# Kernel tuning notes

Hardware: AMD Instinct MI355X
Metric: run time of the kernel (lower is better)

## Reference

```python
import jax, jax.numpy as jnp
import numpy as np

D = 1024          # input_dim == output_dim (module requires this)
H = 4 * D         # expert hidden dim
E = 8             # num_experts
TOP_K = 2
N = 16384         # tokens


def setup_inputs() -> dict:
    key = jax.random.key(0)
    ks = jax.random.split(key, 8)
    s = 0.02
    return {
        "x": jax.random.normal(ks[0], (N, D), dtype=jnp.float32),
        "grad": jax.random.normal(ks[1], (N, 1), dtype=jnp.float32),
        "rW": jax.random.normal(ks[2], (D + 1, E), dtype=jnp.float32) * s,
        "rb": jnp.zeros((E,), dtype=jnp.float32),
        "W1": jax.random.normal(ks[3], (E, D, H), dtype=jnp.float32) * s,
        "b1": jnp.zeros((E, H), dtype=jnp.float32),
        "W2": jax.random.normal(ks[4], (E, H, D), dtype=jnp.float32) * s,
        "b2": jnp.zeros((E, D), dtype=jnp.float32),
    }


def reference(x, grad, rW, rb, W1, b1, W2, b2):
    # Router over [x, grad]
    logits = jnp.concatenate([x, grad], axis=-1) @ rW + rb          # [N, E]
    probs = jax.nn.softmax(logits, axis=-1)                          # [N, E]
    topk_probs, topk_idx = jax.lax.top_k(probs, TOP_K)               # [N, K]
    # Dense gate matrix: gate[n, e] = topk prob if e selected else 0
    gates = jnp.zeros_like(probs).at[jnp.arange(x.shape[0])[:, None], topk_idx].add(topk_probs)
    # Combine: out = sum_e gate_e * MLP_e(x). Dropout is identity at eval.
    out = jnp.zeros((x.shape[0], D), dtype=x.dtype)
    for e in range(E):  # fixed small loop over experts
        h = jax.nn.gelu(x @ W1[e] + b1[e], approximate=False)        # [N, H]
        y = h @ W2[e] + b2[e]                                        # [N, D]
        out = out + gates[:, e:e + 1] * y
    return out, probs
```

## Files before the change

### kernel.cpp

```cpp
#include <hip/hip_runtime.h>
#include <hip/hip_bf16.h>
#include <math.h>

#define NTOK 16384
#define DDIM 1024
#define HDIM 4096
#define NEXP 8

typedef __bf16 bf16_t;
typedef __bf16 bf16x8 __attribute__((ext_vector_type(8)));
typedef float f32x4 __attribute__((ext_vector_type(4)));

__device__ __forceinline__ void gld16(const bf16_t* g, bf16_t* l) {
    __builtin_amdgcn_global_load_lds(
        (const __attribute__((address_space(1))) void*)g,
        (__attribute__((address_space(3))) void*)l, 16, 0, 0);
}

__device__ __forceinline__ void stage_half(const bf16_t* __restrict__ g, int K, int kofs,
                                           bf16_t* l, int tid) {
#pragma unroll
    for (int c = 0; c < 2; ++c) {
        const int s = c * 512 + tid;
        const int kg = s >> 7, r = s & 127;
        gld16(g + (size_t)r * K + (kofs + kg * 8), l + (size_t)s * 8);
    }
}


__global__ void init_counts(int* counts) {
    if (threadIdx.x < NEXP) counts[threadIdx.x] = 0;
}

__global__ void router_kernel(const float* __restrict__ x, const float* __restrict__ grad,
                              const float* __restrict__ rW, const float* __restrict__ rb,
                              float* __restrict__ probs, int* __restrict__ t2i,
                              float* __restrict__ t2g, int* __restrict__ counts) {
    const int lane = threadIdx.x & 63;
    const int n = blockIdx.x * 4 + (threadIdx.x >> 6);
    float acc[NEXP];
#pragma unroll
    for (int e = 0; e < NEXP; ++e) acc[e] = 0.f;
    const float* xr = x + (size_t)n * DDIM;
    for (int d = lane; d < DDIM; d += 64) {
        float xv = xr[d];
        const float* rr = rW + (size_t)d * NEXP;
#pragma unroll
        for (int e = 0; e < NEXP; ++e) acc[e] = fmaf(xv, rr[e], acc[e]);
    }
#pragma unroll
    for (int e = 0; e < NEXP; ++e) {
#pragma unroll
        for (int off = 32; off > 0; off >>= 1)
            acc[e] += __shfl_xor(acc[e], off, 64);
    }
    if (lane == 0) {
        float gv = grad[n];
        float p[NEXP];
        float mx = -1e30f;
#pragma unroll
        for (int e = 0; e < NEXP; ++e) {
            p[e] = acc[e] + gv * rW[(size_t)DDIM * NEXP + e] + rb[e];
            mx = fmaxf(mx, p[e]);
        }
        float s = 0.f;
#pragma unroll
        for (int e = 0; e < NEXP; ++e) { p[e] = expf(p[e] - mx); s += p[e]; }
        float inv = 1.f / s;
        int i1 = 0; float v1 = -1.f;
#pragma unroll
        for (int e = 0; e < NEXP; ++e) {
            p[e] *= inv;
            probs[(size_t)n * NEXP + e] = p[e];
            if (p[e] > v1) { v1 = p[e]; i1 = e; }
        }
        int i2 = 0; float v2 = -2.f;
#pragma unroll
        for (int e = 0; e < NEXP; ++e) {
            if (e != i1 && p[e] > v2) { v2 = p[e]; i2 = e; }
        }
        t2i[n * 2] = i1; t2i[n * 2 + 1] = i2;
        t2g[n * 2] = v1; t2g[n * 2 + 1] = v2;
        atomicAdd(&counts[i1], 1);
        atomicAdd(&counts[i2], 1);
    }
}

__global__ void offsets_kernel(const int* __restrict__ counts, int* __restrict__ offsets,
                               int* __restrict__ cursor) {
    if (threadIdx.x == 0) {
        int s = 0;
        for (int e = 0; e < NEXP; ++e) { offsets[e] = s; cursor[e] = s; s += counts[e]; }
    }
}

__global__ void build_lists(const int* __restrict__ t2i, const float* __restrict__ t2g,
                            int* __restrict__ cursor, int* __restrict__ tok,
                            float* __restrict__ gate, int* __restrict__ tslot) {
    int n = blockIdx.x * 256 + threadIdx.x;
#pragma unroll
    for (int k = 0; k < 2; ++k) {
        int e = t2i[n * 2 + k];
        int slot = atomicAdd(&cursor[e], 1);
        tok[slot] = n;
        gate[slot] = t2g[n * 2 + k];
        tslot[n * 2 + k] = slot;
    }
}

__global__ void gather_kernel(const float* __restrict__ x, const int* __restrict__ tok,
                              bf16_t* __restrict__ Xg) {
    const int r = blockIdx.x;
    const int t = threadIdx.x;
    const int token = tok[r];
    float4 v = ((const float4*)(x + (size_t)token * DDIM))[t];
    bf16_t o[4] = { (bf16_t)v.x, (bf16_t)v.y, (bf16_t)v.z, (bf16_t)v.w };
    *(uint2*)(Xg + (size_t)r * DDIM + t * 4) = *(const uint2*)o;
}

__global__ void transpose_cast(const float* __restrict__ in, bf16_t* __restrict__ out,
                               int R, int C) {
    __shared__ float tile[32][33];
    const size_t ebase = (size_t)blockIdx.z * R * C;
    const int c0 = blockIdx.x * 32, r0 = blockIdx.y * 32;
    const int tx = threadIdx.x, ty = threadIdx.y;
#pragma unroll
    for (int j = 0; j < 32; j += 8)
        tile[ty + j][tx] = in[ebase + (size_t)(r0 + ty + j) * C + c0 + tx];
    __syncthreads();
#pragma unroll
    for (int j = 0; j < 32; j += 8)
        out[ebase + (size_t)(c0 + ty + j) * R + r0 + tx] = (bf16_t)tile[tx][ty + j];
}

__global__ void combine_kernel(const float* __restrict__ Yg, const int* __restrict__ tslot,
                               float* __restrict__ out) {
    const int n = blockIdx.x, t = threadIdx.x;
    const int s1 = tslot[n * 2], s2 = tslot[n * 2 + 1];
    const float4 a = ((const float4*)(Yg + (size_t)s1 * DDIM))[t];
    const float4 b = ((const float4*)(Yg + (size_t)s2 * DDIM))[t];
    ((float4*)(out + (size_t)n * DDIM))[t] =
        make_float4(a.x + b.x, a.y + b.y, a.z + b.z, a.w + b.w);
}

#define PHASE_SYNC() do { \
    __builtin_amdgcn_s_barrier(); \
    asm volatile("s_waitcnt lgkmcnt(0)" ::: "memory"); \
    __builtin_amdgcn_sched_barrier(0); \
    __builtin_amdgcn_s_setprio(1); \
} while (0)

#define PHASE_END() do { \
    __builtin_amdgcn_s_setprio(0); \
    __builtin_amdgcn_s_barrier(); \
} while (0)

#define MMA16(QA, QB) do { \
    _Pragma("unroll") \
    for (int mt = 0; mt < 4; ++mt) { \
        _Pragma("unroll") \
        for (int nt = 0; nt < 2; ++nt) { \
            _Pragma("unroll") \
            for (int ks = 0; ks < 2; ++ks) \
                acc[(QA) * 4 + mt][(QB) * 2 + nt] = \
                    __builtin_amdgcn_mfma_f32_16x16x32_bf16( \
                        aF[mt][ks], bF[nt][ks], acc[(QA) * 4 + mt][(QB) * 2 + nt], 0, 0, 0); \
        } \
    } \
} while (0)

template <int K, int EPI>
__global__ __launch_bounds__(512, 2)
void moe_gemm8(const bf16_t* __restrict__ A, const bf16_t* __restrict__ B,
               const float* __restrict__ bias, bf16_t* __restrict__ Hout,
               float* __restrict__ Yg, const int* __restrict__ counts,
               const int* __restrict__ offsets, const float* __restrict__ gate,
               int gx) {
    const int NT = K / 64;
    const int nwg = gridDim.x;
    const int q8 = nwg >> 3;
    const int v = (blockIdx.x & 7) * q8 + (blockIdx.x >> 3);
    const int per_e = gx * 64;
    const int e = v / per_e;
    const int rem = v - e * per_e;
    const int xsc = gx >> 2;
    const int sup = rem >> 5, sub = rem & 31;
    const int ys = sup / xsc, xs = sup - ys * xsc;
    const int yb = ys * 8 + (sub >> 2), xb = xs * 4 + (sub & 3);

    const int count = counts[e];
    const int m0 = yb * 256;
    if (m0 >= count) return;
    const int n0 = xb * 256;
    const int off = offsets[e];

    const bf16_t* Ae = A + (size_t)(off + m0) * K;
    const bf16_t* Be = B + (size_t)e * HDIM * DDIM + (size_t)n0 * K;
    const bf16_t* Ae1 = Ae + (size_t)128 * K;
    const bf16_t* Be1 = Be + (size_t)128 * K;

    __shared__ __align__(16) bf16_t lds[2][2][2][8192];

    const int tid = threadIdx.x;
    const int lane = tid & 63;
    const int lm = lane & 15, hi = lane >> 4;
    const int wv = tid >> 6;
    const int wm16 = (wv >> 2) << 4;
    const int wn16 = (wv & 3) << 4;

    f32x4 acc[8][4];
    const f32x4 zf = {0.f, 0.f, 0.f, 0.f};
#pragma unroll
    for (int i = 0; i < 8; ++i)
#pragma unroll
        for (int j = 0; j < 4; ++j) acc[i][j] = zf;

    bf16x8 aF[4][2], bF[2][2];
    auto readA = [&](const bf16_t* Ab) {
#pragma unroll
        for (int mt = 0; mt < 4; ++mt)
#pragma unroll
            for (int ks = 0; ks < 2; ++ks)
                aF[mt][ks] = *(const bf16x8*)(Ab + (size_t)((ks * 4 + hi) * 128 +
                                                            mt * 32 + wm16 + lm) * 8);
    };
    auto readB = [&](const bf16_t* Bb) {
#pragma unroll
        for (int nt = 0; nt < 2; ++nt)
#pragma unroll
            for (int ks = 0; ks < 2; ++ks)
                bF[nt][ks] = *(const bf16x8*)(Bb + (size_t)((ks * 4 + hi) * 128 +
                                                            nt * 64 + wn16 + lm) * 8);
    };

    stage_half(Ae,  K, 0, &lds[0][0][0][0], tid);
    stage_half(Ae1, K, 0, &lds[0][0][1][0], tid);
    stage_half(Be,  K, 0, &lds[0][1][0][0], tid);
    stage_half(Be1, K, 0, &lds[0][1][1][0], tid);
    const int k1p = (NT > 1 ? 1 : 0) * 64;
    stage_half(Ae,  K, k1p, &lds[1][0][0][0], tid);
    stage_half(Be1, K, k1p, &lds[1][1][1][0], tid);
    asm volatile("s_waitcnt vmcnt(4)" ::: "memory");
    __builtin_amdgcn_s_barrier();

    int cur = 0;
    for (int t = 0; t < NT; ++t, cur ^= 1) {
        const int nxt = cur ^ 1;
        const int k1 = ((t + 1 < NT) ? t + 1 : NT - 1) * 64;
        const int k2 = ((t + 2 < NT) ? t + 2 : NT - 1) * 64;
        readA(&lds[cur][0][0][0]);
        readB(&lds[cur][1][0][0]);
        stage_half(Ae1, K, k1, &lds[nxt][0][1][0], tid);
        stage_half(Be,  K, k1, &lds[nxt][1][0][0], tid);
        PHASE_SYNC(); MMA16(0, 0); PHASE_END();
        readB(&lds[cur][1][1][0]);
        stage_half(Ae, K, k2, &lds[cur][0][0][0], tid);
        PHASE_SYNC(); MMA16(0, 1); PHASE_END();
        readA(&lds[cur][0][1][0]);
        stage_half(Be1, K, k2, &lds[cur][1][1][0], tid);
        PHASE_SYNC(); MMA16(1, 1); PHASE_END();
        readB(&lds[cur][1][0][0]);
        PHASE_SYNC(); MMA16(1, 0);
        __builtin_amdgcn_s_setprio(0);
        asm volatile("s_waitcnt vmcnt(4)" ::: "memory");
        __builtin_amdgcn_s_barrier();
    }

    if (EPI == 0) {
        const float* bp = bias + (size_t)e * HDIM + n0;
#pragma unroll
        for (int mt = 0; mt < 8; ++mt) {
#pragma unroll
            for (int r = 0; r < 4; ++r) {
                const int row = m0 + mt * 32 + wm16 + hi * 4 + r;
                if (row < count) {
                    bf16_t* hrow = Hout + (size_t)(off + row) * HDIM + n0;
#pragma unroll
                    for (int nt = 0; nt < 4; ++nt) {
                        const int c = nt * 64 + wn16 + lm;
                        float vv = acc[mt][nt][r] + bp[c];
                        hrow[c] = (bf16_t)(0.5f * vv *
                                           (1.f + erff(vv * 0.70710678118654752f)));
                    }
                }
            }
        }
    } else {
        const float* bp = bias + (size_t)e * DDIM + n0;
#pragma unroll
        for (int mt = 0; mt < 8; ++mt) {
#pragma unroll
            for (int r = 0; r < 4; ++r) {
                const int row = m0 + mt * 32 + wm16 + hi * 4 + r;
                if (row < count) {
                    const int slot = off + row;
                    const float g = gate[slot];
                    float* yrow = Yg + (size_t)slot * DDIM + n0;
#pragma unroll
                    for (int nt = 0; nt < 4; ++nt) {
                        const int c = nt * 64 + wn16 + lm;
                        yrow[c] = g * (acc[mt][nt][r] + bp[c]);
                    }
                }
            }
        }
    }
}


extern "C" void kernel_launch(void* const* d_in, const int* in_sizes, int n_in,
                              void* d_out, int out_size, void* d_ws, size_t ws_size,
                              hipStream_t stream) {
    const float* x    = (const float*)d_in[0];
    const float* grad = (const float*)d_in[1];
    const float* rW   = (const float*)d_in[2];
    const float* rb   = (const float*)d_in[3];
    const float* W1   = (const float*)d_in[4];
    const float* b1   = (const float*)d_in[5];
    const float* W2   = (const float*)d_in[6];
    const float* b2   = (const float*)d_in[7];
    float* out   = (float*)d_out;
    float* probs = out + (size_t)NTOK * DDIM;

    char* base = (char*)d_ws;
    size_t p = 0;
    auto alloc = [&](size_t bytes) -> void* {
        void* r = base + p;
        p = (p + bytes + 255) & ~(size_t)255;
        return r;
    };

    int*    counts  = (int*)alloc(3 * NEXP * sizeof(int));
    int*    offsets = counts + NEXP;
    int*    cursor  = offsets + NEXP;
    int*    t2i   = (int*)alloc((size_t)NTOK * 2 * sizeof(int));
    float*  t2g   = (float*)alloc((size_t)NTOK * 2 * sizeof(float));
    int*    tok   = (int*)alloc((size_t)2 * NTOK * sizeof(int));
    float*  gate  = (float*)alloc((size_t)2 * NTOK * sizeof(float));
    int*    tslot = (int*)alloc((size_t)NTOK * 2 * sizeof(int));
    bf16_t* Xg   = (bf16_t*)alloc(((size_t)2 * NTOK + 256) * DDIM * sizeof(bf16_t));
    bf16_t* W1t  = (bf16_t*)alloc((size_t)NEXP * HDIM * DDIM * sizeof(bf16_t));
    bf16_t* W2t  = (bf16_t*)alloc((size_t)NEXP * HDIM * DDIM * sizeof(bf16_t));
    bf16_t* Hbuf = (bf16_t*)alloc(((size_t)2 * NTOK + 256) * HDIM * sizeof(bf16_t));
    float* Yg = (float*)Xg;

    hipLaunchKernelGGL(init_counts, dim3(1), dim3(64), 0, stream, counts);
    hipLaunchKernelGGL(router_kernel, dim3(NTOK / 4), dim3(256), 0, stream,
                       x, grad, rW, rb, probs, t2i, t2g, counts);
    hipLaunchKernelGGL(offsets_kernel, dim3(1), dim3(64), 0, stream, counts, offsets, cursor);
    hipLaunchKernelGGL(build_lists, dim3(NTOK / 256), dim3(256), 0, stream,
                       t2i, t2g, cursor, tok, gate, tslot);
    hipLaunchKernelGGL(gather_kernel, dim3(2 * NTOK), dim3(256), 0, stream, x, tok, Xg);
    hipLaunchKernelGGL(transpose_cast, dim3(HDIM / 32, DDIM / 32, NEXP), dim3(32, 8), 0, stream,
                       W1, W1t, DDIM, HDIM);
    hipLaunchKernelGGL(transpose_cast, dim3(DDIM / 32, HDIM / 32, NEXP), dim3(32, 8), 0, stream,
                       W2, W2t, HDIM, DDIM);

    hipLaunchKernelGGL((moe_gemm8<DDIM, 0>), dim3((HDIM / 256) * 64 * NEXP), dim3(512), 0,
                       stream, Xg, W1t, b1, Hbuf, (float*)nullptr, counts, offsets, gate,
                       HDIM / 256);
    hipLaunchKernelGGL((moe_gemm8<HDIM, 1>), dim3((DDIM / 256) * 64 * NEXP), dim3(512), 0,
                       stream, Hbuf, W2t, b2, (bf16_t*)nullptr, Yg, counts, offsets, gate,
                       DDIM / 256);
    hipLaunchKernelGGL(combine_kernel, dim3(NTOK), dim3(256), 0, stream, Yg, tslot, out);
}
```

Baseline: 2.062 ms.

## Merge weight transposes into one vectorized kernel and use fast erf in GELU

Replaces the two 32x32 weight transpose-cast launches with one kernel over both W1 and W2. It uses 64x64 tiles, float4 global reads and 16-byte bf16 stores, aiming to cut launch count and raise memory efficiency in the weight conversion. The GELU epilogue replaces erff with an Abramowitz-Stegun polynomial built on a hardware reciprocal and fast exp. This makes the epilogue cheaper at a small accuracy cost. The MFMA fragment arrays are also re-indexed, which is mostly cosmetic.

```diff
diff --git a/kernel.cpp b/kernel.cpp
--- a/kernel.cpp
+++ b/kernel.cpp
@@ -25,6 +25,15 @@
         const int kg = s >> 7, r = s & 127;
         gld16(g + (size_t)r * K + (kofs + kg * 8), l + (size_t)s * 8);
     }
+}
+
+__device__ __forceinline__ float erf_fast(float u) {
+    float au = fabsf(u);
+    float tt = __builtin_amdgcn_rcpf(1.f + 0.3275911f * au);
+    float poly = tt * (0.254829592f + tt * (-0.284496736f +
+                 tt * (1.421413741f + tt * (-1.453152027f + tt * 1.061405429f))));
+    float er = 1.f - poly * __expf(-au * au);
+    return (u < 0.f) ? -er : er;
 }
 
 
@@ -118,19 +127,41 @@
     *(uint2*)(Xg + (size_t)r * DDIM + t * 4) = *(const uint2*)o;
 }
 
-__global__ void transpose_cast(const float* __restrict__ in, bf16_t* __restrict__ out,
-                               int R, int C) {
-    __shared__ float tile[32][33];
-    const size_t ebase = (size_t)blockIdx.z * R * C;
-    const int c0 = blockIdx.x * 32, r0 = blockIdx.y * 32;
-    const int tx = threadIdx.x, ty = threadIdx.y;
-#pragma unroll
-    for (int j = 0; j < 32; j += 8)
-        tile[ty + j][tx] = in[ebase + (size_t)(r0 + ty + j) * C + c0 + tx];
+__global__ void transpose_cast2(const float* __restrict__ W1, const float* __restrict__ W2,
+                                bf16_t* __restrict__ W1t, bf16_t* __restrict__ W2t) {
+    __shared__ float tile[64][65];
+    const int z = blockIdx.y;
+    const float* in;
+    bf16_t* out;
+    int R, C;
+    if (z < 8) { in = W1 + (size_t)z * DDIM * HDIM; out = W1t + (size_t)z * DDIM * HDIM;
+                 R = DDIM; C = HDIM; }
+    else       { in = W2 + (size_t)(z - 8) * DDIM * HDIM; out = W2t + (size_t)(z - 8) * DDIM * HDIM;
+                 R = HDIM; C = DDIM; }
+    const int ct = C >> 6;
+    const int c0 = (blockIdx.x & (ct - 1)) << 6;
+    const int r0 = (blockIdx.x / ct) << 6;
+    const int t = threadIdx.x;
+    const int tc = t & 15, tr = t >> 4;
+#pragma unroll
+    for (int i = 0; i < 4; ++i) {
+        const int rr = tr + i * 16;
+        const float4 v = *(const float4*)&in[(size_t)(r0 + rr) * C + c0 + tc * 4];
+        tile[rr][tc * 4 + 0] = v.x;
+        tile[rr][tc * 4 + 1] = v.y;
+        tile[rr][tc * 4 + 2] = v.z;
+        tile[rr][tc * 4 + 3] = v.w;
+    }
     __syncthreads();
-#pragma unroll
-    for (int j = 0; j < 32; j += 8)
-        out[ebase + (size_t)(c0 + ty + j) * R + r0 + tx] = (bf16_t)tile[tx][ty + j];
+    const int oc = t >> 2;
+#pragma unroll
+    for (int i = 0; i < 2; ++i) {
+        const int rb = (t & 3) + i * 4;
+        bf16_t o[8];
+#pragma unroll
+        for (int k = 0; k < 8; ++k) o[k] = (bf16_t)tile[rb * 8 + k][oc];
+        *(uint4*)&out[(size_t)(c0 + oc) * R + r0 + rb * 8] = *(const uint4*)o;
+    }
 }
 
 __global__ void combine_kernel(const float* __restrict__ Yg, const int* __restrict__ tslot,
@@ -164,7 +195,7 @@
             for (int ks = 0; ks < 2; ++ks) \
                 acc[(QA) * 4 + mt][(QB) * 2 + nt] = \
                     __builtin_amdgcn_mfma_f32_16x16x32_bf16( \
-                        aF[mt][ks], bF[nt][ks], acc[(QA) * 4 + mt][(QB) * 2 + nt], 0, 0, 0); \
+                        aF[ks][mt], bF[ks][nt], acc[(QA) * 4 + mt][(QB) * 2 + nt], 0, 0, 0); \
         } \
     } \
 } while (0)
@@ -215,13 +246,13 @@
 #pragma unroll
         for (int j = 0; j < 4; ++j) acc[i][j] = zf;
 
-    bf16x8 aF[4][2], bF[2][2];
+    bf16x8 aF[2][4], bF[2][2];
     auto readA = [&](const bf16_t* Ab) {
 #pragma unroll
         for (int mt = 0; mt < 4; ++mt)
 #pragma unroll
             for (int ks = 0; ks < 2; ++ks)
-                aF[mt][ks] = *(const bf16x8*)(Ab + (size_t)((ks * 4 + hi) * 128 +
+                aF[ks][mt] = *(const bf16x8*)(Ab + (size_t)((ks * 4 + hi) * 128 +
                                                             mt * 32 + wm16 + lm) * 8);
     };
     auto readB = [&](const bf16_t* Bb) {
@@ -229,7 +260,7 @@
         for (int nt = 0; nt < 2; ++nt)
 #pragma unroll
             for (int ks = 0; ks < 2; ++ks)
-                bF[nt][ks] = *(const bf16x8*)(Bb + (size_t)((ks * 4 + hi) * 128 +
+                bF[ks][nt] = *(const bf16x8*)(Bb + (size_t)((ks * 4 + hi) * 128 +
                                                             nt * 64 + wn16 + lm) * 8);
     };
 
@@ -277,10 +308,10 @@
                     bf16_t* hrow = Hout + (size_t)(off + row) * HDIM + n0;
 #pragma unroll
                     for (int nt = 0; nt < 4; ++nt) {
-                        const int c = nt * 64 + wn16 + lm;
-                        float vv = acc[mt][nt][r] + bp[c];
-                        hrow[c] = (bf16_t)(0.5f * vv *
-                                           (1.f + erff(vv * 0.70710678118654752f)));
+                        const int cc = nt * 64 + wn16 + lm;
+                        float vv = acc[mt][nt][r] + bp[cc];
+                        float er = erf_fast(vv * 0.70710678118654752f);
+                        hrow[cc] = (bf16_t)(0.5f * vv * (1.f + er));
                     }
                 }
             }
@@ -298,8 +329,8 @@
                     float* yrow = Yg + (size_t)slot * DDIM + n0;
 #pragma unroll
                     for (int nt = 0; nt < 4; ++nt) {
-                        const int c = nt * 64 + wn16 + lm;
-                        yrow[c] = g * (acc[mt][nt][r] + bp[c]);
+                        const int cc = nt * 64 + wn16 + lm;
+                        yrow[cc] = g * (acc[mt][nt][r] + bp[cc]);
                     }
                 }
             }
@@ -351,10 +382,8 @@
     hipLaunchKernelGGL(build_lists, dim3(NTOK / 256), dim3(256), 0, stream,
                        t2i, t2g, cursor, tok, gate, tslot);
     hipLaunchKernelGGL(gather_kernel, dim3(2 * NTOK), dim3(256), 0, stream, x, tok, Xg);
-    hipLaunchKernelGGL(transpose_cast, dim3(HDIM / 32, DDIM / 32, NEXP), dim3(32, 8), 0, stream,
-                       W1, W1t, DDIM, HDIM);
-    hipLaunchKernelGGL(transpose_cast, dim3(DDIM / 32, HDIM / 32, NEXP), dim3(32, 8), 0, stream,
-                       W2, W2t, HDIM, DDIM);
+    hipLaunchKernelGGL(transpose_cast2, dim3(1024, 16), dim3(256), 0, stream,
+                       W1, W2, W1t, W2t);
 
     hipLaunchKernelGGL((moe_gemm8<DDIM, 0>), dim3((HDIM / 256) * 64 * NEXP), dim3(512), 0,
                        stream, Xg, W1t, b1, Hbuf, (float*)nullptr, counts, offsets, gate,
```

Measured after the change: 1.937 ms. 1.06x faster.
